# Kernel tuning notes

Measured on AMD Instinct MI355X. Metric: run time of the kernel, lower is better.

## Reference

```python
import jax, jax.numpy as jnp
import numpy as np

N_DOMAINS = 4          # number of unique domain labels in d
NUM_PROJ = 50          # hard-coded in DiscriminativeSlicedWasserstein.__init__
P_POW = 2              # hard-coded p=2


def setup_inputs() -> dict:
    key = jax.random.key(0)
    k1, k2, k3 = jax.random.split(key, 3)
    N, IN_DIM, OUT_DIM = 32768, 2048, 512
    z = jax.random.normal(k1, (N, IN_DIM), dtype=jnp.float32)
    W = jax.random.normal(k2, (IN_DIM, OUT_DIM), dtype=jnp.float32) * 0.02
    b = jnp.zeros((OUT_DIM,), dtype=jnp.float32)
    # random projections on the unit sphere (rows normalized), as in rand_projections
    P = jax.random.normal(k3, (NUM_PROJ, OUT_DIM), dtype=jnp.float32)
    P = P / jnp.sqrt(jnp.sum(P * P, axis=1, keepdims=True))
    # sorted, equal-count domain labels -> grouping becomes a static reshape
    d = jnp.repeat(jnp.arange(N_DOMAINS, dtype=jnp.int32), N // N_DOMAINS)
    return {"z": z, "W": W, "b": b, "P": P, "d": d}


def reference(z, W, b, P, d):
    # z = self.D(z): linear discriminator
    h = z @ W + b                                   # [N, out_dim]
    per = h.shape[0] // N_DOMAINS
    groups = h.reshape(N_DOMAINS, per, -1)          # [G, n, out_dim] (d is sorted equal-count)
    # project each group onto the random directions: z.matmul(P.T)
    proj = jnp.einsum('gnd,kd->gnk', groups, P)     # [G, n, num_proj]
    # sort along the sample axis (torch sorts each projection's values)
    srt = jnp.sort(proj, axis=1)                    # [G, n, num_proj]
    # all domain pairs (itertools.combinations); equal group sizes => mean of
    # per-pair means == mean over the stacked pair differences
    ii, jj = np.triu_indices(N_DOMAINS, k=1)
    diff = srt[jj] - srt[ii]                        # [n_pairs, n, num_proj]
    loss = jnp.mean(diff ** P_POW)
    return loss
```

## Files before the change

### kernel.cpp

```cpp
#include <hip/hip_runtime.h>

#define NROWS 32768
#define KDIM  2048
#define DDIM  512
#define NPROJ 50
#define NDOM  4
#define NPER  8192
#define BNPAD 64

typedef __attribute__((ext_vector_type(8))) short short8v;
typedef __attribute__((ext_vector_type(4))) float f32x4;

__device__ inline ushort bf16_rne(float x) {
  union { float f; unsigned u; } v; v.f = x;
  unsigned r = v.u + 0x7FFF + ((v.u >> 16) & 1);
  return (ushort)(r >> 16);
}
__device__ inline float bf16_f32(ushort h) {
  union { unsigned u; float f; } v; v.u = ((unsigned)h) << 16;
  return v.f;
}

__global__ __launch_bounds__(256) void wp_kernel(const float* __restrict__ W,
                                                 const float* __restrict__ b,
                                                 const float* __restrict__ P,
                                                 ushort* __restrict__ Bpk,
                                                 float* __restrict__ bp) {
  int idx = blockIdx.x * 256 + threadIdx.x;
  if (idx >= (KDIM + 1) * BNPAD) return;
  int i = idx >> 6;
  int c = idx & 63;
  float acc = 0.f;
  if (c < NPROJ) {
    const float4* row = (const float4*)((i < KDIM) ? (W + (size_t)i * DDIM) : b);
    const float4* pr  = (const float4*)(P + (size_t)c * DDIM);
#pragma unroll 4
    for (int d = 0; d < DDIM / 4; ++d) {
      float4 w = row[d], p = pr[d];
      acc += w.x * p.x + w.y * p.y + w.z * p.z + w.w * p.w;
    }
  }
  if (i < KDIM) {
    int tg = i >> 5, kb = (i >> 3) & 3, e = i & 7;
    int m = c & 15, cf = c >> 4;
    size_t pos = (size_t)(tg * 4 + cf) * 1024 + (kb * 16 + m) * 8 + e;
    ushort h = bf16_rne(acc);
    Bpk[pos]       = h;
    Bpk[pos + 512] = bf16_rne(acc - bf16_f32(h));
  } else {
    bp[c] = acc;
  }
}

__device__ __forceinline__ void split8_trunc(const float4 f0, const float4 f1,
                                             short8v& hi, short8v& lo) {
  const float a[8] = {f0.x, f0.y, f0.z, f0.w, f1.x, f1.y, f1.z, f1.w};
  union { unsigned u[4]; short8v s; } H, L;
#pragma unroll
  for (int p = 0; p < 4; ++p) {
    float a0 = a[2 * p], a1 = a[2 * p + 1];
    unsigned u0 = __float_as_uint(a0), u1 = __float_as_uint(a1);
    H.u[p] = __builtin_amdgcn_perm(u1, u0, 0x07060302);
    float l0 = a0 - __uint_as_float(u0 & 0xFFFF0000u);
    float l1 = a1 - __uint_as_float(u1 & 0xFFFF0000u);
    L.u[p] = __builtin_amdgcn_perm(__float_as_uint(l1), __float_as_uint(l0), 0x07060302);
  }
  hi = H.s; lo = L.s;
}

__device__ __forceinline__ void gload16(const float* g, float* l) {
  __builtin_amdgcn_global_load_lds(
      (const __attribute__((address_space(1))) unsigned int*)(unsigned long long)g,
      (__attribute__((address_space(3))) unsigned int*)(unsigned int)(unsigned long long)l,
      16, 0, 0);
}

__global__ __launch_bounds__(256) void gemm_mfma(const float* __restrict__ z,
                                                 const ushort* __restrict__ Bpk,
                                                 const float* __restrict__ bp,
                                                 float* __restrict__ projT) {
  __shared__ __align__(16) float A_lds[2][4096];
  __shared__ __align__(16) float B_lds[2][4096];

  const int tid  = threadIdx.x;
  const int lane = tid & 63;
  const int wave = tid >> 6;
  const int m    = lane & 15;
  const int kb   = lane >> 4;
  const int row0 = blockIdx.x * 64;

  const float* gsrcA[4];
  const float* gsrcB[4];
  const float* Bf = (const float*)Bpk;
#pragma unroll
  for (int ii = 0; ii < 4; ++ii) {
    const int i    = wave * 4 + ii;
    const int trow = i * 4 + (lane >> 4);
    const int q    = (lane & 15) ^ (trow & 15);
    gsrcA[ii] = z + (size_t)(row0 + trow) * KDIM + q * 4;
    gsrcB[ii] = Bf + (size_t)i * 256 + lane * 4;
  }

#define STAGE(buf_, t_)                                                  \
  {                                                                      \
    _Pragma("unroll")                                                    \
    for (int ii = 0; ii < 4; ++ii) {                                     \
      const int i = wave * 4 + ii;                                       \
      gload16(gsrcA[ii] + (t_) * 64, &A_lds[buf_][i * 256]);             \
      gload16(gsrcB[ii] + (size_t)(t_) * 4096, &B_lds[buf_][i * 256]);   \
    }                                                                    \
  }

  f32x4 acc[4] = {(f32x4)0.f, (f32x4)0.f, (f32x4)0.f, (f32x4)0.f};

  STAGE(0, 0);
  __syncthreads();

  for (int t = 0; t < 32; ++t) {
    const int buf = t & 1;
    if (t < 31) STAGE(buf ^ 1, t + 1);

    const float* base = &A_lds[buf][(wave * 16 + m) * 64];
    float4 f[2][2];
#pragma unroll
    for (int ks = 0; ks < 2; ++ks) {
      const int q0 = ks * 8 + kb * 2;
      f[ks][0] = *(const float4*)(base + ((q0 ^ m) * 4));
      f[ks][1] = *(const float4*)(base + (((q0 + 1) ^ m) * 4));
    }
    short8v ah[2], al[2];
#pragma unroll
    for (int ks = 0; ks < 2; ++ks)
      split8_trunc(f[ks][0], f[ks][1], ah[ks], al[ks]);

    const ushort* Bu = (const ushort*)&B_lds[buf][0];
#pragma unroll
    for (int ks = 0; ks < 2; ++ks) {
#pragma unroll
      for (int cf = 0; cf < 4; ++cf) {
        const ushort* fb = Bu + (ks * 4 + cf) * 1024 + lane * 8;
        short8v bh = *(const short8v*)fb;
        short8v bl = *(const short8v*)(fb + 512);
        acc[cf] = __builtin_amdgcn_mfma_f32_16x16x32_bf16(ah[ks], bh, acc[cf], 0, 0, 0);
        acc[cf] = __builtin_amdgcn_mfma_f32_16x16x32_bf16(al[ks], bh, acc[cf], 0, 0, 0);
        acc[cf] = __builtin_amdgcn_mfma_f32_16x16x32_bf16(ah[ks], bl, acc[cf], 0, 0, 0);
      }
    }
    __syncthreads();
  }
#undef STAGE

  const int g     = row0 >> 13;
  const int nbase = (row0 & (NPER - 1)) + wave * 16;
#pragma unroll
  for (int cf = 0; cf < 4; ++cf) {
    const int col = cf * 16 + m;
    if (col < NPROJ) {
      const float bj = bp[col];
      float* dst = projT + (size_t)(g * NPROJ + col) * NPER + nbase + kb * 4;
      dst[0] = acc[cf][0] + bj;
      dst[1] = acc[cf][1] + bj;
      dst[2] = acc[cf][2] + bj;
      dst[3] = acc[cf][3] + bj;
    }
  }
}

#define CE(a, b, asc) { float x_ = v[a], y_ = v[b]; \
  if ((asc) ? (x_ > y_) : (x_ < y_)) { v[a] = y_; v[b] = x_; } }

__device__ inline int swz(int i) { return i ^ (((i >> 5) & 7) << 2); }
#define SPAD 8192

template <int JMAX>
__device__ inline void wave_merge(float v[8], int t, int k) {
  const bool asc = (((t << 3) & k) == 0);
#pragma unroll
  for (int j = JMAX; j >= 8; j >>= 1) {
    const int d = j >> 3;
    const bool keepmin = (asc != ((t & d) != 0));
#pragma unroll
    for (int e = 0; e < 8; ++e) {
      float o = __shfl_xor(v[e], d, 64);
      v[e] = keepmin ? fminf(v[e], o) : fmaxf(v[e], o);
    }
  }
  CE(0, 4, asc); CE(1, 5, asc); CE(2, 6, asc); CE(3, 7, asc);
  CE(0, 2, asc); CE(1, 3, asc); CE(4, 6, asc); CE(5, 7, asc);
  CE(0, 1, asc); CE(2, 3, asc); CE(4, 5, asc); CE(6, 7, asc);
}

__global__ __launch_bounds__(1024) void sort_cols(float* __restrict__ projT) {
  __shared__ __align__(16) float sA[SPAD];
  __shared__ __align__(16) float sB[SPAD];
  float* col = projT + (size_t)blockIdx.x * NPER;
  const int t  = threadIdx.x;
  const int i0 = t << 3;
  float v[8];

  *(float4*)&v[0] = *(const float4*)(col + i0);
  *(float4*)&v[4] = *(const float4*)(col + i0 + 4);

  CE(0, 1, true);  CE(2, 3, false); CE(4, 5, true);  CE(6, 7, false);
  CE(0, 2, true);  CE(1, 3, true);  CE(4, 6, false); CE(5, 7, false);
  CE(0, 1, true);  CE(2, 3, true);  CE(4, 5, false); CE(6, 7, false);
  {
    bool d8 = (t & 1) == 0;
    CE(0, 4, d8); CE(1, 5, d8); CE(2, 6, d8); CE(3, 7, d8);
    CE(0, 2, d8); CE(1, 3, d8); CE(4, 6, d8); CE(5, 7, d8);
    CE(0, 1, d8); CE(2, 3, d8); CE(4, 5, d8); CE(6, 7, d8);
  }

  wave_merge<8>(v, t, 16);
  wave_merge<16>(v, t, 32);
  wave_merge<32>(v, t, 64);
  wave_merge<64>(v, t, 128);
  wave_merge<128>(v, t, 256);
  wave_merge<256>(v, t, 512);

  *(float4*)&sA[swz(i0)]     = *(float4*)&v[0];
  *(float4*)&sA[swz(i0 + 4)] = *(float4*)&v[4];
  __syncthreads();
  int cur = 0;

  for (int k = 1024; k <= NPER; k <<= 1) {
    const bool asc = ((i0 & k) == 0);
    for (int j = k >> 1; j >= 512; j >>= 1) {
      const float* src = cur ? sB : sA;
      float*       dst = cur ? sA : sB;
      const int ip = i0 ^ j;
      float4 a0 = *(const float4*)&src[swz(i0)];
      float4 a1 = *(const float4*)&src[swz(i0 + 4)];
      float4 b0 = *(const float4*)&src[swz(ip)];
      float4 b1 = *(const float4*)&src[swz(ip + 4)];
      const bool keepmin = (asc != ((i0 & j) != 0));
      float4 r0, r1;
      if (keepmin) {
        r0.x = fminf(a0.x, b0.x); r0.y = fminf(a0.y, b0.y); r0.z = fminf(a0.z, b0.z); r0.w = fminf(a0.w, b0.w);
        r1.x = fminf(a1.x, b1.x); r1.y = fminf(a1.y, b1.y); r1.z = fminf(a1.z, b1.z); r1.w = fminf(a1.w, b1.w);
      } else {
        r0.x = fmaxf(a0.x, b0.x); r0.y = fmaxf(a0.y, b0.y); r0.z = fmaxf(a0.z, b0.z); r0.w = fmaxf(a0.w, b0.w);
        r1.x = fmaxf(a1.x, b1.x); r1.y = fmaxf(a1.y, b1.y); r1.z = fmaxf(a1.z, b1.z); r1.w = fmaxf(a1.w, b1.w);
      }
      *(float4*)&dst[swz(i0)]     = r0;
      *(float4*)&dst[swz(i0 + 4)] = r1;
      __syncthreads();
      cur ^= 1;
      *(float4*)&v[0] = r0;
      *(float4*)&v[4] = r1;
    }
    wave_merge<256>(v, t, k);
    if (k != NPER) {
      float* d2 = cur ? sB : sA;
      *(float4*)&d2[swz(i0)]     = *(float4*)&v[0];
      *(float4*)&d2[swz(i0 + 4)] = *(float4*)&v[4];
      __syncthreads();
    }
  }

  *(float4*)(col + i0)     = *(float4*)&v[0];
  *(float4*)(col + i0 + 4) = *(float4*)&v[4];
}

__global__ __launch_bounds__(256) void reduce_k(const float* __restrict__ projT,
                                                float* __restrict__ partial) {
  const int k  = blockIdx.x;
  const int nc = blockIdx.y;
  const int n  = nc * 1024 + threadIdx.x * 4;
  const float4 x0 = *(const float4*)(projT + (size_t)(0 * NPROJ + k) * NPER + n);
  const float4 x1 = *(const float4*)(projT + (size_t)(1 * NPROJ + k) * NPER + n);
  const float4 x2 = *(const float4*)(projT + (size_t)(2 * NPROJ + k) * NPER + n);
  const float4 x3 = *(const float4*)(projT + (size_t)(3 * NPROJ + k) * NPER + n);
  const float a0[4] = {x0.x, x0.y, x0.z, x0.w};
  const float a1[4] = {x1.x, x1.y, x1.z, x1.w};
  const float a2[4] = {x2.x, x2.y, x2.z, x2.w};
  const float a3[4] = {x3.x, x3.y, x3.z, x3.w};
  float local = 0.f;
#pragma unroll
  for (int e = 0; e < 4; ++e) {
    float d01 = a0[e] - a1[e], d02 = a0[e] - a2[e], d03 = a0[e] - a3[e];
    float d12 = a1[e] - a2[e], d13 = a1[e] - a3[e], d23 = a2[e] - a3[e];
    local += d01 * d01 + d02 * d02 + d03 * d03 + d12 * d12 + d13 * d13 + d23 * d23;
  }
#pragma unroll
  for (int o = 32; o > 0; o >>= 1) local += __shfl_down(local, o, 64);
  __shared__ float red[4];
  if ((threadIdx.x & 63) == 0) red[threadIdx.x >> 6] = local;
  __syncthreads();
  if (threadIdx.x == 0) partial[nc * NPROJ + k] = red[0] + red[1] + red[2] + red[3];
}

__global__ __launch_bounds__(512) void final_k(const float* __restrict__ partial,
                                               float* __restrict__ out) {
  const int t = threadIdx.x;
  float v = (t < 8 * NPROJ) ? partial[t] : 0.f;
#pragma unroll
  for (int o = 32; o > 0; o >>= 1) v += __shfl_down(v, o, 64);
  __shared__ float red[8];
  if ((t & 63) == 0) red[t >> 6] = v;
  __syncthreads();
  if (t == 0) {
    float s = 0.f;
#pragma unroll
    for (int w = 0; w < 8; ++w) s += red[w];
    out[0] = s * (1.0f / (6.0f * NPER * NPROJ));
  }
}

extern "C" void kernel_launch(void* const* d_in, const int* in_sizes, int n_in,
                              void* d_out, int out_size, void* d_ws, size_t ws_size,
                              hipStream_t stream) {
  const float* z = (const float*)d_in[0];
  const float* W = (const float*)d_in[1];
  const float* b = (const float*)d_in[2];
  const float* P = (const float*)d_in[3];

  float*  projT   = (float*)d_ws;
  ushort* Bpk     = (ushort*)(projT + (size_t)NDOM * NPROJ * NPER);
  float*  bp      = (float*)(Bpk + (size_t)2 * BNPAD * KDIM);
  float*  partial = bp + BNPAD;

  wp_kernel<<<((KDIM + 1) * BNPAD + 255) / 256, 256, 0, stream>>>(W, b, P, Bpk, bp);
  gemm_mfma<<<NROWS / 64, 256, 0, stream>>>(z, Bpk, bp, projT);
  sort_cols<<<NDOM * NPROJ, 1024, 0, stream>>>(projT);
  reduce_k<<<dim3(NPROJ, 8), 256, 0, stream>>>(projT, partial);
  final_k<<<1, 512, 0, stream>>>(partial, (float*)d_out);
}
```

Baseline: 128.5 us.

## Split GEMM over K into four slices and sum partials in sort kernel

The projection GEMM now runs on a 2D grid: 32-row tiles times four K-slices of 512. Each block loads its A slice into LDS once and reads the packed B operand straight from global memory instead of double-buffering it through LDS. Two waves per row-half reduce through LDS, and each K-slice writes its own partial buffer, which the sort kernel sums on load. This adds parallelism and removes the per-step barrier pipeline, at the cost of extra partial-buffer traffic and uncached global B reads.

```diff
diff --git a/kernel.cpp b/kernel.cpp
--- a/kernel.cpp
+++ b/kernel.cpp
@@ -7,6 +7,7 @@
 #define NDOM  4
 #define NPER  8192
 #define BNPAD 64
+#define PELEM ((size_t)NDOM * NPROJ * NPER)
 
 typedef __attribute__((ext_vector_type(8))) short short8v;
 typedef __attribute__((ext_vector_type(4))) float f32x4;
@@ -78,90 +79,71 @@
 __global__ __launch_bounds__(256) void gemm_mfma(const float* __restrict__ z,
                                                  const ushort* __restrict__ Bpk,
                                                  const float* __restrict__ bp,
-                                                 float* __restrict__ projT) {
-  __shared__ __align__(16) float A_lds[2][4096];
-  __shared__ __align__(16) float B_lds[2][4096];
+                                                 float* __restrict__ part) {
+  __shared__ __align__(16) float A_lds[4][16 * 256];
+  __shared__ __align__(16) f32x4 red[2][4][64];
 
   const int tid  = threadIdx.x;
   const int lane = tid & 63;
   const int wave = tid >> 6;
+  const int rh   = wave & 1;
+  const int kq   = wave >> 1;
   const int m    = lane & 15;
   const int kb   = lane >> 4;
-  const int row0 = blockIdx.x * 64;
-
-  const float* gsrcA[4];
-  const float* gsrcB[4];
-  const float* Bf = (const float*)Bpk;
-#pragma unroll
-  for (int ii = 0; ii < 4; ++ii) {
-    const int i    = wave * 4 + ii;
-    const int trow = i * 4 + (lane >> 4);
-    const int q    = (lane & 15) ^ (trow & 15);
-    gsrcA[ii] = z + (size_t)(row0 + trow) * KDIM + q * 4;
-    gsrcB[ii] = Bf + (size_t)i * 256 + lane * 4;
-  }
-
-#define STAGE(buf_, t_)                                                  \
-  {                                                                      \
-    _Pragma("unroll")                                                    \
-    for (int ii = 0; ii < 4; ++ii) {                                     \
-      const int i = wave * 4 + ii;                                       \
-      gload16(gsrcA[ii] + (t_) * 64, &A_lds[buf_][i * 256]);             \
-      gload16(gsrcB[ii] + (size_t)(t_) * 4096, &B_lds[buf_][i * 256]);   \
-    }                                                                    \
-  }
+  const int row0 = blockIdx.x * 32;
+  const int ksb  = blockIdx.y;
+  const int k0   = ksb * 512 + kq * 256;
+
+#pragma unroll
+  for (int i = 0; i < 16; ++i) {
+    const int r = row0 + rh * 16 + i;
+    gload16(z + (size_t)r * KDIM + k0 + ((lane ^ i) << 2), &A_lds[wave][i * 256]);
+  }
+  __syncthreads();
 
   f32x4 acc[4] = {(f32x4)0.f, (f32x4)0.f, (f32x4)0.f, (f32x4)0.f};
-
-  STAGE(0, 0);
-  __syncthreads();
-
-  for (int t = 0; t < 32; ++t) {
-    const int buf = t & 1;
-    if (t < 31) STAGE(buf ^ 1, t + 1);
-
-    const float* base = &A_lds[buf][(wave * 16 + m) * 64];
-    float4 f[2][2];
-#pragma unroll
-    for (int ks = 0; ks < 2; ++ks) {
-      const int q0 = ks * 8 + kb * 2;
-      f[ks][0] = *(const float4*)(base + ((q0 ^ m) * 4));
-      f[ks][1] = *(const float4*)(base + (((q0 + 1) ^ m) * 4));
-    }
-    short8v ah[2], al[2];
-#pragma unroll
-    for (int ks = 0; ks < 2; ++ks)
-      split8_trunc(f[ks][0], f[ks][1], ah[ks], al[ks]);
-
-    const ushort* Bu = (const ushort*)&B_lds[buf][0];
-#pragma unroll
-    for (int ks = 0; ks < 2; ++ks) {
-#pragma unroll
-      for (int cf = 0; cf < 4; ++cf) {
-        const ushort* fb = Bu + (ks * 4 + cf) * 1024 + lane * 8;
-        short8v bh = *(const short8v*)fb;
-        short8v bl = *(const short8v*)(fb + 512);
-        acc[cf] = __builtin_amdgcn_mfma_f32_16x16x32_bf16(ah[ks], bh, acc[cf], 0, 0, 0);
-        acc[cf] = __builtin_amdgcn_mfma_f32_16x16x32_bf16(al[ks], bh, acc[cf], 0, 0, 0);
-        acc[cf] = __builtin_amdgcn_mfma_f32_16x16x32_bf16(ah[ks], bl, acc[cf], 0, 0, 0);
+  const int tgbase = k0 >> 5;
+  const float* base = &A_lds[wave][m * 256];
+
+#pragma unroll 2
+  for (int t = 0; t < 8; ++t) {
+    const int c0 = t * 8 + kb * 2;
+    float4 f0 = *(const float4*)(base + (((c0)     ^ m) << 2));
+    float4 f1 = *(const float4*)(base + (((c0 + 1) ^ m) << 2));
+    short8v ah, al;
+    split8_trunc(f0, f1, ah, al);
+#pragma unroll
+    for (int cf = 0; cf < 4; ++cf) {
+      const ushort* fb = Bpk + (size_t)((tgbase + t) * 4 + cf) * 1024 + lane * 8;
+      short8v bh = *(const short8v*)fb;
+      short8v bl = *(const short8v*)(fb + 512);
+      acc[cf] = __builtin_amdgcn_mfma_f32_16x16x32_bf16(ah, bh, acc[cf], 0, 0, 0);
+      acc[cf] = __builtin_amdgcn_mfma_f32_16x16x32_bf16(al, bh, acc[cf], 0, 0, 0);
+      acc[cf] = __builtin_amdgcn_mfma_f32_16x16x32_bf16(ah, bl, acc[cf], 0, 0, 0);
+    }
+  }
+
+  if (kq == 1) {
+#pragma unroll
+    for (int cf = 0; cf < 4; ++cf) red[rh][cf][lane] = acc[cf];
+  }
+  __syncthreads();
+  if (kq == 0) {
+    const int g     = row0 >> 13;
+    const int nbase = (row0 & (NPER - 1)) + rh * 16 + kb * 4;
+#pragma unroll
+    for (int cf = 0; cf < 4; ++cf) {
+      const int col = cf * 16 + m;
+      if (col < NPROJ) {
+        f32x4 s = acc[cf] + red[rh][cf][lane];
+        const float bj = (ksb == 0) ? bp[col] : 0.f;
+        float* dst = part + (size_t)ksb * PELEM +
+                     (size_t)(g * NPROJ + col) * NPER + nbase;
+        dst[0] = s[0] + bj;
+        dst[1] = s[1] + bj;
+        dst[2] = s[2] + bj;
+        dst[3] = s[3] + bj;
       }
-    }
-    __syncthreads();
-  }
-#undef STAGE
-
-  const int g     = row0 >> 13;
-  const int nbase = (row0 & (NPER - 1)) + wave * 16;
-#pragma unroll
-  for (int cf = 0; cf < 4; ++cf) {
-    const int col = cf * 16 + m;
-    if (col < NPROJ) {
-      const float bj = bp[col];
-      float* dst = projT + (size_t)(g * NPROJ + col) * NPER + nbase + kb * 4;
-      dst[0] = acc[cf][0] + bj;
-      dst[1] = acc[cf][1] + bj;
-      dst[2] = acc[cf][2] + bj;
-      dst[3] = acc[cf][3] + bj;
     }
   }
 }
@@ -190,16 +172,31 @@
   CE(0, 1, asc); CE(2, 3, asc); CE(4, 5, asc); CE(6, 7, asc);
 }
 
-__global__ __launch_bounds__(1024) void sort_cols(float* __restrict__ projT) {
+__global__ __launch_bounds__(1024) void sort_cols(float* __restrict__ p0,
+                                                  const float* __restrict__ p1,
+                                                  const float* __restrict__ p2,
+                                                  const float* __restrict__ p3) {
   __shared__ __align__(16) float sA[SPAD];
   __shared__ __align__(16) float sB[SPAD];
-  float* col = projT + (size_t)blockIdx.x * NPER;
+  float* col = p0 + (size_t)blockIdx.x * NPER;
   const int t  = threadIdx.x;
   const int i0 = t << 3;
   float v[8];
 
   *(float4*)&v[0] = *(const float4*)(col + i0);
   *(float4*)&v[4] = *(const float4*)(col + i0 + 4);
+  {
+    const float* c1 = p1 + (size_t)blockIdx.x * NPER;
+    const float* c2 = p2 + (size_t)blockIdx.x * NPER;
+    const float* c3 = p3 + (size_t)blockIdx.x * NPER;
+    float4 a0 = *(const float4*)(c1 + i0), a1 = *(const float4*)(c1 + i0 + 4);
+    float4 b0 = *(const float4*)(c2 + i0), b1 = *(const float4*)(c2 + i0 + 4);
+    float4 d0 = *(const float4*)(c3 + i0), d1 = *(const float4*)(c3 + i0 + 4);
+    v[0] += a0.x + b0.x + d0.x; v[1] += a0.y + b0.y + d0.y;
+    v[2] += a0.z + b0.z + d0.z; v[3] += a0.w + b0.w + d0.w;
+    v[4] += a1.x + b1.x + d1.x; v[5] += a1.y + b1.y + d1.y;
+    v[6] += a1.z + b1.z + d1.z; v[7] += a1.w + b1.w + d1.w;
+  }
 
   CE(0, 1, true);  CE(2, 3, false); CE(4, 5, true);  CE(6, 7, false);
   CE(0, 2, true);  CE(1, 3, true);  CE(4, 6, false); CE(5, 7, false);
@@ -315,14 +312,17 @@
   const float* b = (const float*)d_in[2];
   const float* P = (const float*)d_in[3];
 
-  float*  projT   = (float*)d_ws;
-  ushort* Bpk     = (ushort*)(projT + (size_t)NDOM * NPROJ * NPER);
+  float*  part0   = (float*)d_ws;
+  float*  part1   = part0 + PELEM;
+  float*  part2   = part1 + PELEM;
+  float*  part3   = part2 + PELEM;
+  ushort* Bpk     = (ushort*)(part3 + PELEM);
   float*  bp      = (float*)(Bpk + (size_t)2 * BNPAD * KDIM);
   float*  partial = bp + BNPAD;
 
   wp_kernel<<<((KDIM + 1) * BNPAD + 255) / 256, 256, 0, stream>>>(W, b, P, Bpk, bp);
-  gemm_mfma<<<NROWS / 64, 256, 0, stream>>>(z, Bpk, bp, projT);
-  sort_cols<<<NDOM * NPROJ, 1024, 0, stream>>>(projT);
-  reduce_k<<<dim3(NPROJ, 8), 256, 0, stream>>>(projT, partial);
+  gemm_mfma<<<dim3(NROWS / 32, 4), 256, 0, stream>>>(z, Bpk, bp, part0);
+  sort_cols<<<NDOM * NPROJ, 1024, 0, stream>>>(part0, part1, part2, part3);
+  reduce_k<<<dim3(NPROJ, 8), 256, 0, stream>>>(part0, partial);
   final_k<<<1, 512, 0, stream>>>(partial, (float*)d_out);
 }
```

Measured after the change: 183.4 us. 42.7% more time.
